# Kernel optimization log

Measured on AMD Instinct MI355X. Metric: run time of the kernel, lower is better.

The kernel has to match this reference:

```python
import jax, jax.numpy as jnp
import numpy as np

TAU = 1.0
K_ROUTE = 3
EPS = 1e-8


def setup_inputs() -> dict:
    key = jax.random.key(0)
    ks = jax.random.split(key, 8)
    B, T, D_in, H, D_out, L, d_addr = 8, 8192, 1024, 1024, 1024, 12, 64

    def unit_rows(k, L_, d_):
        U = jax.random.normal(k, (L_, d_), dtype=jnp.float32)
        U = U - U.mean(axis=1, keepdims=True)
        return U / (jnp.linalg.norm(U, axis=1, keepdims=True) + EPS)

    def norm_tape(k, shape):
        W = jax.random.normal(k, shape, dtype=jnp.float32)
        # F.normalize over last two dims per expert
        n = jnp.sqrt(jnp.sum(W * W, axis=tuple(range(1, W.ndim)), keepdims=True)) + 1e-12
        return W / n

    x = jax.random.normal(ks[0], (B, T, D_in), dtype=jnp.float32)
    P_w = jax.random.normal(ks[1], (d_addr, D_in), dtype=jnp.float32) / np.sqrt(D_in)
    U1 = unit_rows(ks[2], L, d_addr)
    U2 = unit_rows(ks[3], L, d_addr)
    U3 = unit_rows(ks[4], L, d_addr)
    W1 = norm_tape(ks[5], (L, H, D_in))
    W2 = norm_tape(ks[6], (L, D_out, H))
    b2 = norm_tape(ks[7], (L, D_out))
    return {"x": x, "P_w": P_w, "U1": U1, "U2": U2, "U3": U3,
            "W1": W1, "W2": W2, "b2": b2}


def _route_combine_weights(x_addr, U, k, tau):
    """Top-k routing -> dense combine matrix C: [N, L], zero off the top-k.
    Mathematically identical to scattering softmax(topv/tau) onto expert slots,
    matching RouterTopK.forward + the grouped dispatch/combine."""
    z = x_addr @ U.T                      # [N, L]
    topv, topi = jax.lax.top_k(z, k)      # [N, k]
    w = jax.nn.softmax(topv / (tau + EPS), axis=1)
    N, L = z.shape
    rows = jnp.arange(N)[:, None]
    return jnp.zeros((N, L), z.dtype).at[rows, topi].add(w)


def _mixture(inp, C, W):
    """y[n] = sum_e C[n,e] * (W[e] @ inp[n]); C is top-k sparse per row.
    Loop over the small fixed expert count L (12) with one dense GEMM each;
    equals _apply_mixture_grouped since C is zero for unselected experts."""
    L = W.shape[0]
    y = jnp.zeros((inp.shape[0], W.shape[1]), inp.dtype)
    for e in range(L):
        y = y + C[:, e:e + 1] * (inp @ W[e].T)
    return y


def reference(x, P_w, U1, U2, U3, W1, W2, b2):
    B, T, D = x.shape
    xf = x.reshape(B * T, D)              # [N, D_in]
    xa = xf @ P_w.T                       # [N, d_addr]
    C1 = _route_combine_weights(xa, U1, K_ROUTE, TAU)
    C2 = _route_combine_weights(xa, U2, K_ROUTE, TAU)
    C3 = _route_combine_weights(xa, U3, K_ROUTE, TAU)
    h = jax.nn.gelu(_mixture(xf, C1, W1), approximate=False)  # nn.GELU (exact)
    y = _mixture(h, C2, W2) + C3 @ b2      # routed bias == _apply_bias_grouped
    return y.reshape(B, T, -1)
```

## Files before the change

### kernel.cpp

```cpp
#include <hip/hip_runtime.h>

#define NTOT 65536

typedef __attribute__((ext_vector_type(8))) short bf16x8;
typedef __attribute__((ext_vector_type(4))) float f32x4;

__device__ __forceinline__ float bf2f(unsigned short u) {
    union { unsigned int i; float f; } v; v.i = ((unsigned int)u) << 16; return v.f;
}
__device__ __forceinline__ unsigned short f2bf(float f) {
    union { float f; unsigned int i; } v; v.f = f;
    unsigned int i = v.i;
    return (unsigned short)((i + 0x7FFFu + ((i >> 16) & 1u)) >> 16);
}
__device__ __forceinline__ float lo16(unsigned int v) { return bf2f((unsigned short)(v & 0xFFFFu)); }
__device__ __forceinline__ float hi16(unsigned int v) { return bf2f((unsigned short)(v >> 16)); }

__device__ __forceinline__ void gload16(const void* g, void* l) {
    __builtin_amdgcn_global_load_lds((const __attribute__((address_space(1))) void*)(g),
                                     (__attribute__((address_space(3))) void*)(l), 16, 0, 0);
}

__global__ __launch_bounds__(256) void cvt_bf16(const float* __restrict__ src,
                                                unsigned short* __restrict__ dst) {
    size_t i = ((size_t)blockIdx.x * 256 + threadIdx.x) * 8;
    float4 a = *(const float4*)(src + i);
    float4 b = *(const float4*)(src + i + 4);
    unsigned int o0 = (unsigned int)f2bf(a.x) | ((unsigned int)f2bf(a.y) << 16);
    unsigned int o1 = (unsigned int)f2bf(a.z) | ((unsigned int)f2bf(a.w) << 16);
    unsigned int o2 = (unsigned int)f2bf(b.x) | ((unsigned int)f2bf(b.y) << 16);
    unsigned int o3 = (unsigned int)f2bf(b.z) | ((unsigned int)f2bf(b.w) << 16);
    uint4 o = {o0, o1, o2, o3};
    *(uint4*)(dst + i) = o;
}

__global__ void zero_counts(int* c1, int* c2) {
    if (threadIdx.x < 16) { c1[threadIdx.x] = 0; c2[threadIdx.x] = 0; }
}

__global__ __launch_bounds__(256) void compute_M(const float* __restrict__ U1,
                                                 const float* __restrict__ U2,
                                                 const float* __restrict__ U3,
                                                 const float* __restrict__ Pw,
                                                 double* __restrict__ M) {
    int le = blockIdx.x;
    int l = le / 12, e = le % 12;
    const float* U = (l == 0 ? U1 : (l == 1 ? U2 : U3)) + e * 64;
    int c = threadIdx.x * 4;
    double a0 = 0.0, a1 = 0.0, a2 = 0.0, a3 = 0.0;
    for (int a = 0; a < 64; a++) {
        double u = (double)U[a];
        float4 p = *(const float4*)&Pw[(size_t)a * 1024 + c];
        a0 += u * (double)p.x; a1 += u * (double)p.y;
        a2 += u * (double)p.z; a3 += u * (double)p.w;
    }
    double* mp = M + (size_t)le * 1024 + c;
    mp[0] = a0; mp[1] = a1; mp[2] = a2; mp[3] = a3;
}

__global__ __launch_bounds__(256) void z_gemm(const float* __restrict__ X,
                                              const double* __restrict__ Mg,
                                              double* __restrict__ z, int tok_base) {
    __shared__ __align__(16) float xs[128 * 64];
    __shared__ __align__(16) double Ms[36 * 64];
    const int tid = threadIdx.x;
    const int w = tid >> 6, lane = tid & 63;
    const int tok0 = tid & 63, tok1 = tok0 + 64;
    const int eg = tid >> 6;
    const int tb = blockIdx.x * 128;

    double acc[2][9];
#pragma unroll
    for (int t = 0; t < 2; t++)
#pragma unroll
        for (int j = 0; j < 9; j++) acc[t][j] = 0.0;

    for (int kc = 0; kc < 16; ++kc) {
        int k0 = kc * 64;
        for (int i = w; i < 50; i += 4) {
            if (i < 32) {
                int r = i * 4 + (lane >> 4);
                int p = lane & 15;
                const float* g = X + (size_t)(tok_base + tb + r) * 1024 + k0 + ((p ^ (r & 7)) << 2);
                gload16(g, xs + i * 256 + lane * 4);
            } else {
                int ii = i - 32;
                int e = ii * 2 + (lane >> 5);
                const double* g = Mg + (size_t)e * 1024 + k0 + ((lane & 31) << 1);
                gload16(g, Ms + ii * 128 + lane * 2);
            }
        }
        __syncthreads();
#pragma unroll
        for (int kq = 0; kq < 16; ++kq) {
            int p = (kq ^ (tok0 & 7)) << 2;
            float4 xa4 = *(const float4*)&xs[(tok0 << 6) + p];
            float4 xb4 = *(const float4*)&xs[(tok1 << 6) + p];
            double xd00 = (double)xa4.x, xd01 = (double)xa4.y,
                   xd02 = (double)xa4.z, xd03 = (double)xa4.w;
            double xd10 = (double)xb4.x, xd11 = (double)xb4.y,
                   xd12 = (double)xb4.z, xd13 = (double)xb4.w;
            const double* mp = &Ms[(eg * 9) * 64 + (kq << 2)];
#pragma unroll
            for (int j = 0; j < 9; j++) {
                double2 m0 = *(const double2*)(mp + j * 64);
                double2 m1 = *(const double2*)(mp + j * 64 + 2);
                acc[0][j] += xd00 * m0.x + xd01 * m0.y + xd02 * m1.x + xd03 * m1.y;
                acc[1][j] += xd10 * m0.x + xd11 * m0.y + xd12 * m1.x + xd13 * m1.y;
            }
        }
        __syncthreads();
    }
    double* zp0 = z + (size_t)(tb + tok0) * 36 + eg * 9;
    double* zp1 = z + (size_t)(tb + tok1) * 36 + eg * 9;
#pragma unroll
    for (int j = 0; j < 9; j++) { zp0[j] = acc[0][j]; zp1[j] = acc[1][j]; }
}

__global__ __launch_bounds__(256) void route2(
    const double* __restrict__ z,
    int* __restrict__ counts1, int* __restrict__ counts2,
    int* __restrict__ bucket1, float* __restrict__ bucketw1,
    int* __restrict__ bucket2, float* __restrict__ bucketw2,
    int* __restrict__ topi3, float* __restrict__ topw3, int Nc) {
    __shared__ int lcnt1[12], lcnt2[12], gbase1[12], gbase2[12];
    int tid = threadIdx.x;
    if (tid < 12) { lcnt1[tid] = 0; lcnt2[tid] = 0; }
    __syncthreads();
    int n = blockIdx.x * 256 + tid;
    int ei[3][3]; float ew[3][3];
    for (int l = 0; l < 3; l++) {
        double zz[12];
        const double* zp = z + (size_t)n * 36 + l * 12;
#pragma unroll
        for (int e = 0; e < 12; e += 2) {
            double2 v = *(const double2*)(zp + e);
            zz[e] = v.x; zz[e + 1] = v.y;
        }
        int i0 = 0, i1 = 0, i2 = 0; double v0 = -1e300, v1 = -1e300, v2 = -1e300;
#pragma unroll
        for (int e = 0; e < 12; e++) {
            double v = zz[e];
            if (v > v0)      { v2 = v1; i2 = i1; v1 = v0; i1 = i0; v0 = v; i0 = e; }
            else if (v > v1) { v2 = v1; i2 = i1; v1 = v; i1 = e; }
            else if (v > v2) { v2 = v; i2 = e; }
        }
        float inv = 1.0f / (1.0f + 1e-8f);
        float e1 = expf((float)(v1 - v0) * inv), e2 = expf((float)(v2 - v0) * inv);
        float s = 1.0f + e1 + e2;
        ew[l][0] = 1.0f / s; ew[l][1] = e1 / s; ew[l][2] = e2 / s;
        ei[l][0] = i0; ei[l][1] = i1; ei[l][2] = i2;
    }
    int lpos1[3], lpos2[3];
    for (int s = 0; s < 3; s++) {
        lpos1[s] = atomicAdd(&lcnt1[ei[0][s]], 1);
        lpos2[s] = atomicAdd(&lcnt2[ei[1][s]], 1);
    }
    __syncthreads();
    if (tid < 12) {
        gbase1[tid] = atomicAdd(&counts1[tid], lcnt1[tid]);
        gbase2[tid] = atomicAdd(&counts2[tid], lcnt2[tid]);
    }
    __syncthreads();
    for (int s = 0; s < 3; s++) {
        int e = ei[0][s]; int pos = gbase1[e] + lpos1[s];
        bucket1[e * Nc + pos] = (s << 16) | n;
        bucketw1[e * Nc + pos] = ew[0][s];
        e = ei[1][s]; pos = gbase2[e] + lpos2[s];
        bucket2[e * Nc + pos] = (s << 16) | n;
        bucketw2[e * Nc + pos] = ew[1][s];
        topi3[n * 3 + s] = ei[2][s];
        topw3[n * 3 + s] = ew[2][s];
    }
}

__global__ __launch_bounds__(256) void grouped_gemm(
    const unsigned short* __restrict__ A,
    const unsigned short* __restrict__ W,
    const int* __restrict__ bucket, const float* __restrict__ bucketw,
    const int* __restrict__ counts,
    unsigned short* __restrict__ part, int Nc) {
    __shared__ unsigned short As[128 * 32];
    __shared__ unsigned short Bs[128 * 32];
    __shared__ int ids[128];
    __shared__ float wts[128];
    int bx = blockIdx.x;
    int e = -1, mt = 0, accum = 0, Me = 0;
    for (int ee = 0; ee < 12; ee++) {
        int c = counts[ee];
        int t = (c + 127) >> 7;
        if (e < 0 && bx < accum + t) { e = ee; mt = bx - accum; Me = c; }
        accum += t;
    }
    if (e < 0) return;
    int nt = blockIdx.y;
    int tid = threadIdx.x, lane = tid & 63, w = tid >> 6;
    int m0 = mt << 7;
    if (tid < 128) {
        int r = m0 + tid; if (r >= Me) r = Me - 1;
        ids[tid] = bucket[e * Nc + r];
        wts[tid] = bucketw[e * Nc + r];
    }
    __syncthreads();
    int seg = lane & 3;
    int rA0 = w * 16 + (lane >> 2);
    int rA1 = rA0 + 64;
    const unsigned short* a0p = A + (size_t)(ids[rA0] & 0xFFFF) * 1024 + seg * 8;
    const unsigned short* a1p = A + (size_t)(ids[rA1] & 0xFFFF) * 1024 + seg * 8;
    const unsigned short* b0p = W + (size_t)e * 1048576 + (size_t)(nt * 128 + rA0) * 1024 + seg * 8;
    const unsigned short* b1p = W + (size_t)e * 1048576 + (size_t)(nt * 128 + rA1) * 1024 + seg * 8;
    unsigned short* AsL0 = &As[w * 512 + lane * 8];
    unsigned short* AsL1 = &As[(w + 4) * 512 + lane * 8];
    unsigned short* BsL0 = &Bs[w * 512 + lane * 8];
    unsigned short* BsL1 = &Bs[(w + 4) * 512 + lane * 8];
    f32x4 acc[4][4];
    for (int i = 0; i < 4; i++) for (int j = 0; j < 4; j++) acc[i][j] = (f32x4){0.f, 0.f, 0.f, 0.f};
    int wr0 = (w & 1) * 64, wc0 = (w >> 1) * 64;
    for (int it = 0; it < 32; ++it) {
        int k0 = it * 32;
        gload16(a0p + k0, AsL0);
        gload16(a1p + k0, AsL1);
        gload16(b0p + k0, BsL0);
        gload16(b1p + k0, BsL1);
        __syncthreads();
        int q = lane >> 4, l15 = lane & 15;
        bf16x8 af[4], bfr[4];
        for (int i = 0; i < 4; i++) af[i]  = *(const bf16x8*)&As[(wr0 + i * 16 + l15) * 32 + q * 8];
        for (int j = 0; j < 4; j++) bfr[j] = *(const bf16x8*)&Bs[(wc0 + j * 16 + l15) * 32 + q * 8];
        for (int i = 0; i < 4; i++)
            for (int j = 0; j < 4; j++)
                acc[i][j] = __builtin_amdgcn_mfma_f32_16x16x32_bf16(af[i], bfr[j], acc[i][j], 0, 0, 0);
        __syncthreads();
    }
    int q = lane >> 4, l15 = lane & 15;
    for (int i = 0; i < 4; i++) {
        for (int r = 0; r < 4; r++) {
            int row = wr0 + i * 16 + q * 4 + r;
            if (m0 + row >= Me) continue;
            int id = ids[row];
            int n = id & 0xFFFF, slot = id >> 16;
            float wt = wts[row];
            size_t base = ((size_t)slot * Nc + n) * 1024 + (size_t)(nt * 128 + wc0);
            for (int j = 0; j < 4; j++)
                part[base + j * 16 + l15] = f2bf(acc[i][j][r] * wt);
        }
    }
}

__global__ __launch_bounds__(256) void combine_gelu(const unsigned short* __restrict__ part,
                                                    unsigned short* __restrict__ h, int Nc) {
    size_t idx = ((size_t)blockIdx.x * 256 + threadIdx.x) * 8;
    const size_t S = (size_t)Nc * 1024;
    uint4 a = *(const uint4*)(part + idx);
    uint4 b = *(const uint4*)(part + S + idx);
    uint4 c = *(const uint4*)(part + 2 * S + idx);
    unsigned int pa[4] = {a.x, a.y, a.z, a.w};
    unsigned int pb[4] = {b.x, b.y, b.z, b.w};
    unsigned int pc[4] = {c.x, c.y, c.z, c.w};
    unsigned int po[4];
    for (int k = 0; k < 4; k++) {
        float s0 = lo16(pa[k]) + lo16(pb[k]) + lo16(pc[k]);
        float s1 = hi16(pa[k]) + hi16(pb[k]) + hi16(pc[k]);
        float g0 = 0.5f * s0 * (1.0f + erff(s0 * 0.70710678118654752f));
        float g1 = 0.5f * s1 * (1.0f + erff(s1 * 0.70710678118654752f));
        po[k] = (unsigned int)f2bf(g0) | ((unsigned int)f2bf(g1) << 16);
    }
    uint4 o = {po[0], po[1], po[2], po[3]};
    *(uint4*)(h + idx) = o;
}

__global__ __launch_bounds__(256) void final_out(const unsigned short* __restrict__ part,
                                                 const int* __restrict__ topi3,
                                                 const float* __restrict__ topw3,
                                                 const float* __restrict__ b2,
                                                 float* __restrict__ out, int Nc) {
    size_t idx = ((size_t)blockIdx.x * 256 + threadIdx.x) * 8;
    const size_t S = (size_t)Nc * 1024;
    int n = (int)(idx >> 10), col = (int)(idx & 1023);
    uint4 a = *(const uint4*)(part + idx);
    uint4 b = *(const uint4*)(part + S + idx);
    uint4 c = *(const uint4*)(part + 2 * S + idx);
    int e0 = topi3[n * 3 + 0], e1 = topi3[n * 3 + 1], e2 = topi3[n * 3 + 2];
    float w0 = topw3[n * 3 + 0], w1 = topw3[n * 3 + 1], w2 = topw3[n * 3 + 2];
    unsigned int pa[4] = {a.x, a.y, a.z, a.w};
    unsigned int pb[4] = {b.x, b.y, b.z, b.w};
    unsigned int pc[4] = {c.x, c.y, c.z, c.w};
    float r[8];
    for (int k = 0; k < 4; k++) {
        r[2 * k]     = lo16(pa[k]) + lo16(pb[k]) + lo16(pc[k]);
        r[2 * k + 1] = hi16(pa[k]) + hi16(pb[k]) + hi16(pc[k]);
    }
    const float* q0 = b2 + (size_t)e0 * 1024 + col;
    const float* q1 = b2 + (size_t)e1 * 1024 + col;
    const float* q2 = b2 + (size_t)e2 * 1024 + col;
    float4 q0a = *(const float4*)q0, q0b = *(const float4*)(q0 + 4);
    float4 q1a = *(const float4*)q1, q1b = *(const float4*)(q1 + 4);
    float4 q2a = *(const float4*)q2, q2b = *(const float4*)(q2 + 4);
    float bz[8] = {q0a.x * w0 + q1a.x * w1 + q2a.x * w2, q0a.y * w0 + q1a.y * w1 + q2a.y * w2,
                   q0a.z * w0 + q1a.z * w1 + q2a.z * w2, q0a.w * w0 + q1a.w * w1 + q2a.w * w2,
                   q0b.x * w0 + q1b.x * w1 + q2b.x * w2, q0b.y * w0 + q1b.y * w1 + q2b.y * w2,
                   q0b.z * w0 + q1b.z * w1 + q2b.z * w2, q0b.w * w0 + q1b.w * w1 + q2b.w * w2};
    float4 o0 = {r[0] + bz[0], r[1] + bz[1], r[2] + bz[2], r[3] + bz[3]};
    float4 o1 = {r[4] + bz[4], r[5] + bz[5], r[6] + bz[6], r[7] + bz[7]};
    *(float4*)(out + idx) = o0;
    *(float4*)(out + idx + 4) = o1;
}

struct WsPlan {
    size_t w1b, w2b, xb, m, z, c1, c2, bk1, bw1, bk2, bw2, ti, tw, h, part, total;
};
static WsPlan plan_ws(size_t Nc) {
    auto al = [](size_t x) { return (x + 255) & ~(size_t)255; };
    WsPlan p; size_t o = 0;
    p.w1b = o; o = al(o + (size_t)12 * 1024 * 1024 * 2);
    p.w2b = o; o = al(o + (size_t)12 * 1024 * 1024 * 2);
    p.xb  = o; o = al(o + Nc * 1024 * 2);
    p.m   = o; o = al(o + (size_t)36 * 1024 * 8);
    p.z   = o; o = al(o + Nc * 36 * 8);
    p.c1  = o; o = al(o + 64);
    p.c2  = o; o = al(o + 64);
    p.bk1 = o; o = al(o + 12 * Nc * 4);
    p.bw1 = o; o = al(o + 12 * Nc * 4);
    p.bk2 = o; o = al(o + 12 * Nc * 4);
    p.bw2 = o; o = al(o + 12 * Nc * 4);
    p.ti  = o; o = al(o + Nc * 3 * 4);
    p.tw  = o; o = al(o + Nc * 3 * 4);
    p.h   = o; o = al(o + Nc * 1024 * 2);
    p.part= o; o = al(o + (size_t)3 * Nc * 1024 * 2);
    p.total = o;
    return p;
}

extern "C" void kernel_launch(void* const* d_in, const int* in_sizes, int n_in,
                              void* d_out, int out_size, void* d_ws, size_t ws_size,
                              hipStream_t stream) {
    const float* X  = (const float*)d_in[0];
    const float* Pw = (const float*)d_in[1];
    const float* U1 = (const float*)d_in[2];
    const float* U2 = (const float*)d_in[3];
    const float* U3 = (const float*)d_in[4];
    const float* W1 = (const float*)d_in[5];
    const float* W2 = (const float*)d_in[6];
    const float* B2 = (const float*)d_in[7];
    float* OUT = (float*)d_out;

    int C = 1;
    while (C < 64 && plan_ws(NTOT / C).total > ws_size) C <<= 1;
    int Nc = NTOT / C;
    WsPlan p = plan_ws((size_t)Nc);

    char* ws = (char*)d_ws;
    unsigned short* W1b  = (unsigned short*)(ws + p.w1b);
    unsigned short* W2b  = (unsigned short*)(ws + p.w2b);
    unsigned short* Xb   = (unsigned short*)(ws + p.xb);
    double* Md      = (double*)(ws + p.m);
    double* zbuf    = (double*)(ws + p.z);
    int* counts1    = (int*)(ws + p.c1);
    int* counts2    = (int*)(ws + p.c2);
    int* bucket1    = (int*)(ws + p.bk1);
    float* bucketw1 = (float*)(ws + p.bw1);
    int* bucket2    = (int*)(ws + p.bk2);
    float* bucketw2 = (float*)(ws + p.bw2);
    int* topi3      = (int*)(ws + p.ti);
    float* topw3    = (float*)(ws + p.tw);
    unsigned short* h    = (unsigned short*)(ws + p.h);
    unsigned short* part = (unsigned short*)(ws + p.part);

    cvt_bf16<<<6144, 256, 0, stream>>>(W1, W1b);
    cvt_bf16<<<6144, 256, 0, stream>>>(W2, W2b);
    compute_M<<<36, 256, 0, stream>>>(U1, U2, U3, Pw, Md);

    int gg_tiles = 3 * Nc / 128 + 12;
    for (int c = 0; c < C; ++c) {
        int base = c * Nc;
        zero_counts<<<1, 64, 0, stream>>>(counts1, counts2);
        cvt_bf16<<<Nc / 2, 256, 0, stream>>>(X + (size_t)base * 1024, Xb);
        z_gemm<<<Nc / 128, 256, 0, stream>>>(X, Md, zbuf, base);
        route2<<<Nc / 256, 256, 0, stream>>>(zbuf, counts1, counts2,
                                             bucket1, bucketw1, bucket2, bucketw2,
                                             topi3, topw3, Nc);
        grouped_gemm<<<dim3(gg_tiles, 8), 256, 0, stream>>>(Xb, W1b,
                                                            bucket1, bucketw1, counts1, part, Nc);
        combine_gelu<<<Nc / 2, 256, 0, stream>>>(part, h, Nc);
        grouped_gemm<<<dim3(gg_tiles, 8), 256, 0, stream>>>(h, W2b,
                                                            bucket2, bucketw2, counts2, part, Nc);
        final_out<<<Nc / 2, 256, 0, stream>>>(part, topi3, topw3, B2,
                                              OUT + (size_t)base * 1024, Nc);
    }
}
```

Measured before the change: 2.075 ms.

## Pipeline grouped GEMM with 4-stage LDS ring, swizzled layout, and register double-buffering

Rewrites the grouped GEMM main loop so global-to-LDS async loads run three tiles ahead in a 4-buffer ring, gated by explicit vmcnt waits and a single barrier per step instead of two. LDS fragments are prefetched into alternating register sets while MFMAs on the previous set run at raised wave priority. The LDS layout is XOR-swizzled to avoid bank conflicts on fragment reads. Launch bounds now request 2 blocks per CU. The cost is more LDS and more registers, and the hand-counted waitcnt/barrier sequencing is fragile.

```diff
diff --git a/kernel.cpp b/kernel.cpp
--- a/kernel.cpp
+++ b/kernel.cpp
@@ -174,14 +174,44 @@
     }
 }
 
-__global__ __launch_bounds__(256) void grouped_gemm(
+__device__ __forceinline__ void gg_mm(const bf16x8 (&fa)[4], const bf16x8 (&fb)[4],
+                                      f32x4 (&acc)[4][4]) {
+    __builtin_amdgcn_s_setprio(1);
+#pragma unroll
+    for (int i = 0; i < 4; i++)
+#pragma unroll
+        for (int j = 0; j < 4; j++)
+            acc[i][j] = __builtin_amdgcn_mfma_f32_16x16x32_bf16(fa[i], fb[j], acc[i][j], 0, 0, 0);
+    __builtin_amdgcn_s_setprio(0);
+}
+
+#define GG_WAITV(N) asm volatile("s_waitcnt vmcnt(" #N ")" ::: "memory")
+#define GG_WAITL()  asm volatile("s_waitcnt lgkmcnt(0)" ::: "memory")
+#define GG_BAR()    { __builtin_amdgcn_s_barrier(); __builtin_amdgcn_sched_barrier(0); }
+
+#define GG_STG(BUF, KT)                                            \
+    { int kk = (KT) * 32;                                          \
+      gload16(a0p + kk, &As[BUF][dst0]);                           \
+      gload16(a1p + kk, &As[BUF][dst1]);                           \
+      gload16(b0p + kk, &Bs[BUF][dst0]);                           \
+      gload16(b1p + kk, &Bs[BUF][dst1]); }
+
+#define GG_LDA(FA, FB, BUF)                                                        \
+    { _Pragma("unroll")                                                            \
+      for (int i = 0; i < 4; i++)                                                  \
+          FA[i] = *(const bf16x8*)(Abase + (BUF) * 8192 + aoff + i * 1024);        \
+      _Pragma("unroll")                                                            \
+      for (int j = 0; j < 4; j++)                                                  \
+          FB[j] = *(const bf16x8*)(Bbase + (BUF) * 8192 + boff + j * 1024); }
+
+__global__ __launch_bounds__(256, 2) void grouped_gemm(
     const unsigned short* __restrict__ A,
     const unsigned short* __restrict__ W,
     const int* __restrict__ bucket, const float* __restrict__ bucketw,
     const int* __restrict__ counts,
     unsigned short* __restrict__ part, int Nc) {
-    __shared__ unsigned short As[128 * 32];
-    __shared__ unsigned short Bs[128 * 32];
+    __shared__ unsigned short As[4][4096];
+    __shared__ unsigned short Bs[4][4096];
     __shared__ int ids[128];
     __shared__ float wts[128];
     int bx = blockIdx.x;
@@ -202,37 +232,49 @@
         wts[tid] = bucketw[e * Nc + r];
     }
     __syncthreads();
-    int seg = lane & 3;
-    int rA0 = w * 16 + (lane >> 2);
-    int rA1 = rA0 + 64;
-    const unsigned short* a0p = A + (size_t)(ids[rA0] & 0xFFFF) * 1024 + seg * 8;
-    const unsigned short* a1p = A + (size_t)(ids[rA1] & 0xFFFF) * 1024 + seg * 8;
-    const unsigned short* b0p = W + (size_t)e * 1048576 + (size_t)(nt * 128 + rA0) * 1024 + seg * 8;
-    const unsigned short* b1p = W + (size_t)e * 1048576 + (size_t)(nt * 128 + rA1) * 1024 + seg * 8;
-    unsigned short* AsL0 = &As[w * 512 + lane * 8];
-    unsigned short* AsL1 = &As[(w + 4) * 512 + lane * 8];
-    unsigned short* BsL0 = &Bs[w * 512 + lane * 8];
-    unsigned short* BsL1 = &Bs[(w + 4) * 512 + lane * 8];
+
+    int u    = (lane & 7) ^ (lane >> 3);
+    int lr   = w * 16 + ((lane >> 3) << 1) + (u & 1);
+    int cofs = (u >> 1) * 8;
+    const unsigned short* a0p = A + (size_t)(ids[lr] & 0xFFFF) * 1024 + cofs;
+    const unsigned short* a1p = A + (size_t)(ids[lr + 64] & 0xFFFF) * 1024 + cofs;
+    const unsigned short* b0p = W + (size_t)e * 1048576 + (size_t)(nt * 128 + lr) * 1024 + cofs;
+    const unsigned short* b1p = W + (size_t)e * 1048576 + (size_t)(nt * 128 + lr + 64) * 1024 + cofs;
+    int dst0 = w * 512 + lane * 8;
+    int dst1 = 2048 + dst0;
+
+    int q = lane >> 4, l15 = lane & 15;
+    int fo = ((l15 >> 1) * 128) + ((((q << 1) + (l15 & 1)) ^ ((l15 >> 1) & 7)) << 4);
+    int wr0 = (w & 1) * 64, wc0 = (w >> 1) * 64;
+    const char* Abase = (const char*)&As[0][0];
+    const char* Bbase = (const char*)&Bs[0][0];
+    int aoff = wr0 * 64 + fo;
+    int boff = wc0 * 64 + fo;
+
     f32x4 acc[4][4];
-    for (int i = 0; i < 4; i++) for (int j = 0; j < 4; j++) acc[i][j] = (f32x4){0.f, 0.f, 0.f, 0.f};
-    int wr0 = (w & 1) * 64, wc0 = (w >> 1) * 64;
-    for (int it = 0; it < 32; ++it) {
-        int k0 = it * 32;
-        gload16(a0p + k0, AsL0);
-        gload16(a1p + k0, AsL1);
-        gload16(b0p + k0, BsL0);
-        gload16(b1p + k0, BsL1);
-        __syncthreads();
-        int q = lane >> 4, l15 = lane & 15;
-        bf16x8 af[4], bfr[4];
-        for (int i = 0; i < 4; i++) af[i]  = *(const bf16x8*)&As[(wr0 + i * 16 + l15) * 32 + q * 8];
-        for (int j = 0; j < 4; j++) bfr[j] = *(const bf16x8*)&Bs[(wc0 + j * 16 + l15) * 32 + q * 8];
-        for (int i = 0; i < 4; i++)
-            for (int j = 0; j < 4; j++)
-                acc[i][j] = __builtin_amdgcn_mfma_f32_16x16x32_bf16(af[i], bfr[j], acc[i][j], 0, 0, 0);
-        __syncthreads();
-    }
-    int q = lane >> 4, l15 = lane & 15;
+#pragma unroll
+    for (int i = 0; i < 4; i++)
+#pragma unroll
+        for (int j = 0; j < 4; j++) acc[i][j] = (f32x4){0.f, 0.f, 0.f, 0.f};
+
+    bf16x8 fa0[4], fb0[4], fa1[4], fb1[4];
+
+    GG_STG(0, 0); GG_STG(1, 1); GG_STG(2, 2);
+    GG_WAITV(8); GG_BAR();
+    GG_LDA(fa0, fb0, 0);
+    GG_WAITL();
+
+    for (int t4 = 0; t4 < 28; t4 += 4) {
+        GG_STG(3, t4 + 3); GG_WAITV(8); GG_BAR(); GG_LDA(fa1, fb1, 1); gg_mm(fa0, fb0, acc); GG_WAITL();
+        GG_STG(0, t4 + 4); GG_WAITV(8); GG_BAR(); GG_LDA(fa0, fb0, 2); gg_mm(fa1, fb1, acc); GG_WAITL();
+        GG_STG(1, t4 + 5); GG_WAITV(8); GG_BAR(); GG_LDA(fa1, fb1, 3); gg_mm(fa0, fb0, acc); GG_WAITL();
+        GG_STG(2, t4 + 6); GG_WAITV(8); GG_BAR(); GG_LDA(fa0, fb0, 0); gg_mm(fa1, fb1, acc); GG_WAITL();
+    }
+    GG_STG(3, 31); GG_WAITV(8); GG_BAR(); GG_LDA(fa1, fb1, 1); gg_mm(fa0, fb0, acc); GG_WAITL();
+    GG_WAITV(4);  GG_BAR(); GG_LDA(fa0, fb0, 2); gg_mm(fa1, fb1, acc); GG_WAITL();
+    GG_WAITV(0);  GG_BAR(); GG_LDA(fa1, fb1, 3); gg_mm(fa0, fb0, acc); GG_WAITL();
+    gg_mm(fa1, fb1, acc);
+
     for (int i = 0; i < 4; i++) {
         for (int r = 0; r < 4; r++) {
             int row = wr0 + i * 16 + q * 4 + r;
```

After: 2.159 ms. 1.04x slower.
